# Optimization experiments

Hardware: AMD Instinct MI355X
Metric: run time of the kernel (lower is better)

Reference implementation:

```python
import jax, jax.numpy as jnp
import numpy as np

WSIZE = 8
HEADS = 6
CYC_SHIFT = True


def _relative_index(w):
    # same math as SelfAttention._getRelativeIndex
    coords = np.stack(np.meshgrid(np.arange(w), np.arange(w), indexing='ij'))
    coords = coords.reshape(2, -1)                      # [2, w*w]
    rel = coords[:, :, None] - coords[:, None, :]       # [2, N, N]
    rel = rel.copy()
    rel[0] += w - 1
    rel[0] *= 2 * w - 1
    rel[1] += w - 1
    return (rel[0] + rel[1]).reshape(-1)                # [N*N]


def _shift_mask(H, W, w):
    # same math as CycShftWndwPartition._mask
    part = np.zeros((H, W), dtype=np.float32)
    slices = [slice(0, -w), slice(-w, -w // 2), slice(-w // 2, None)]
    idx = 0
    for hs in slices:
        for ws_ in slices:
            part[hs, ws_] = idx
            idx += 1
    part = part.reshape(H // w, w, W // w, w).transpose(0, 2, 1, 3).reshape(-1, w * w)
    diff = part[:, None, :] - part[:, :, None]          # [nW, N, N]
    return np.where(diff != 0, -100.0, 0.0).astype(np.float32)


def setup_inputs() -> dict:
    key = jax.random.key(0)
    k0, k1, k2, k3, k4 = jax.random.split(key, 5)
    B, H, W, C = 4, 384, 384, 60
    return {
        'cvrt_img': jax.random.normal(k0, (B, H, W, C), dtype=jnp.float32),
        'qkv_w': jax.random.normal(k1, (C, 3 * C), dtype=jnp.float32) * 0.05,
        'bias_matrix': jax.random.normal(k2, ((2 * WSIZE - 1) ** 2, HEADS), dtype=jnp.float32) * 0.02,
        'proj_w': jax.random.normal(k3, (C, C), dtype=jnp.float32) * 0.05,
        'proj_b': jax.random.normal(k4, (C,), dtype=jnp.float32) * 0.02,
    }


def reference(cvrt_img, qkv_w, bias_matrix, proj_w, proj_b):
    B, H, W, C = cvrt_img.shape
    w = WSIZE
    N = w * w
    d = C // HEADS
    nWh, nWw = H // w, W // w
    WNum = nWh * nWw

    # cyclic shift + window partition
    if CYC_SHIFT:
        x = jnp.roll(cvrt_img, shift=(-(w // 2), -(w // 2)), axis=(1, 2))
        mask = jnp.asarray(_shift_mask(H, W, w))        # [WNum, N, N]
    else:
        x = cvrt_img
        mask = jnp.zeros((WNum, N, N), dtype=cvrt_img.dtype)
    windows = x.reshape(B, nWh, w, nWw, w, C).transpose(0, 1, 3, 2, 4, 5)
    windows = windows.reshape(B * WNum, N, C)

    # windowed multi-head self-attention
    qkv = (windows @ qkv_w).reshape(B * WNum, N, 3, HEADS, d)
    qkv = qkv.transpose(2, 0, 3, 1, 4)                  # [3, Bw, H, N, d]
    q, k, v = qkv[0], qkv[1], qkv[2]
    attn = jnp.einsum('bhnd,bhmd->bhnm', q, k) / (d ** 0.5)

    rel_idx = jnp.asarray(_relative_index(w))
    bias = bias_matrix[rel_idx].reshape(N, N, HEADS).transpose(2, 0, 1)  # [H, N, N]
    attn = attn + bias[None]

    attn = attn.reshape(B, WNum, HEADS, N, N) + mask[None, :, None]
    attn = jax.nn.softmax(attn.reshape(B * WNum, HEADS, N, N), axis=-1)

    out = jnp.einsum('bhnm,bhmd->bhnd', attn, v)        # [Bw, H, N, d]
    out = out.transpose(0, 2, 1, 3).reshape(B * WNum, N, C)
    new_windows = out @ proj_w + proj_b

    # un-partition + reverse cyclic shift
    y = new_windows.reshape(B, nWh, nWw, w, w, C).transpose(0, 1, 3, 2, 4, 5)
    y = y.reshape(B, H, W, C)
    if CYC_SHIFT:
        y = jnp.roll(y, shift=(w // 2, w // 2), axis=(1, 2))
    return y
```

## Files before the change

### kernel.cpp

```cpp
#include <hip/hip_runtime.h>
#include <hip/hip_bf16.h>

#define IMG    384
#define CDIM   60
#define NWIN   48
#define WNUM   (NWIN * NWIN)

typedef short  bf16x8 __attribute__((ext_vector_type(8)));
typedef float  f32x4  __attribute__((ext_vector_type(4)));
union Frag { int4 i4; bf16x8 b8; };

#define MFMA(a, b, c) __builtin_amdgcn_mfma_f32_16x16x32_bf16((a), (b), (c), 0, 0, 0)

#define WS_QKVF  0
#define WS_VF    24576
#define WS_PROJF 36864
#define WS_BIASC 45056

#define SCALE_L2E (0.31622776601683794f * 1.4426950408889634f)
#define MASK_L2E  144.26950408889634f
#define LOG2E     1.4426950408889634f

__device__ __forceinline__ unsigned short f2bf(float f) {
    unsigned int u = __float_as_uint(f);
    unsigned int r = u + 0x7fffu + ((u >> 16) & 1u);
    return (unsigned short)(r >> 16);
}
__device__ __forceinline__ unsigned int pk2bf(float a, float b) {
    union { __hip_bfloat162 h; unsigned int u; } c;
    c.h = __float22bfloat162_rn(float2{a, b});
    return c.u;
}
__device__ __forceinline__ int regionOf(int x) {
    return (x < IMG - 8) ? 0 : ((x < IMG - 4) ? 1 : 2);
}
__device__ __forceinline__ int swz(int row, int byteoff) {
    return (row * 128 + byteoff) ^ ((row & 7) << 4);
}
__device__ __forceinline__ int4 qk_frag(const unsigned short* buf, int tok, int h, int g) {
    if (g == 0) return *(const int4*)((const char*)buf + swz(tok, h * 16));
    if (g == 1) {
        int v = *(const int*)((const char*)buf + swz(tok, 96 + h * 4));
        return int4{v, 0, 0, 0};
    }
    return int4{0, 0, 0, 0};
}

template<int MC>
__device__ __forceinline__ void attn_group(
    int h, int m0, const Frag (&kb)[4],
    int lane, int l15, int g, int dl, bool boundary, int wh, int ww,
    const unsigned short* qall, const unsigned short* vall,
    unsigned short* osb,
    char* slab, int prow, const float4* biasC)
{
    Frag va[2];
    int vrow = (l15 < 10) ? h * 10 + l15 : 60;
    #pragma unroll
    for (int ks = 0; ks < 2; ++ks)
        va[ks].i4 = *(const int4*)((const char*)vall + swz(vrow, ks * 64 + g * 16));

    #pragma unroll
    for (int mm = 0; mm < MC; ++mm) {
        int m = m0 + mm;
        int i_tok = m * 16 + l15;
        Frag qa;
        qa.i4 = qk_frag(qall, i_tok, h, g);

        const float4* bc = biasC + (h * 16 + m * 4) * 64 + lane;
        f32x4 sacc[4];
        #pragma unroll
        for (int n = 0; n < 4; ++n) {
            float4 bb = bc[n * 64];
            f32x4 ci = {bb.x, bb.y, bb.z, bb.w};
            sacc[n] = MFMA(kb[n].b8, qa.b8, ci);
        }
        if (boundary) {
            int pi = regionOf(wh * 8 + (i_tok >> 3)) * 3 + regionOf(ww * 8 + (i_tok & 7));
            #pragma unroll
            for (int n = 0; n < 4; ++n)
                #pragma unroll
                for (int jj = 0; jj < 4; ++jj) {
                    int j = n * 16 + g * 4 + jj;
                    int pj = regionOf(wh * 8 + (j >> 3)) * 3 + regionOf(ww * 8 + (j & 7));
                    if (pi != pj) sacc[n][jj] -= MASK_L2E;
                }
        }
        unsigned w0[4], w1[4];
        #pragma unroll
        for (int n = 0; n < 4; ++n) {
            float e0 = __builtin_exp2f(sacc[n][0]);
            float e1 = __builtin_exp2f(sacc[n][1]);
            float e2 = __builtin_exp2f(sacc[n][2]);
            float e3 = __builtin_exp2f(sacc[n][3]);
            w0[n] = pk2bf(e0, e1);
            w1[n] = pk2bf(e2, e3);
        }
        f32x4 pv = {0.f, 0.f, 0.f, 0.f};
        *(int2*)(slab + swz(prow, 0 * 32 + g * 8)) = make_int2(w0[0], w1[0]);
        *(int2*)(slab + swz(prow, 1 * 32 + g * 8)) = make_int2(w0[1], w1[1]);
        {
            Frag pf;
            pf.i4 = *(const int4*)(slab + swz(prow, g * 16));
            pv = MFMA(va[0].b8, pf.b8, pv);
        }
        *(int2*)(slab + swz(prow, 0 * 32 + g * 8)) = make_int2(w0[2], w1[2]);
        *(int2*)(slab + swz(prow, 1 * 32 + g * 8)) = make_int2(w0[3], w1[3]);
        {
            Frag pf;
            pf.i4 = *(const int4*)(slab + swz(prow, g * 16));
            pv = MFMA(va[1].b8, pf.b8, pv);
        }
        float denom = __int_as_float(__builtin_amdgcn_ds_bpermute(dl, __float_as_int(pv[2])));
        float rinv  = __builtin_amdgcn_rcpf(denom);

        unsigned q01 = pk2bf(pv[0] * rinv, pv[1] * rinv);
        unsigned q23 = pk2bf(pv[2] * rinv, pv[3] * rinv);
        if (g < 2) {
            *(unsigned*)((char*)osb + swz(i_tok, h * 20 + g * 8 + 0)) = q01;
            *(unsigned*)((char*)osb + swz(i_tok, h * 20 + g * 8 + 4)) = q23;
        } else if (g == 2) {
            *(unsigned*)((char*)osb + swz(i_tok, h * 20 + 16)) = q01;
        }
    }
}

__global__ void swin_prep(const float* __restrict__ qw,
                          const float* __restrict__ pw,
                          const float* __restrict__ bias,
                          unsigned char* __restrict__ ws)
{
    int t = blockIdx.x * 256 + threadIdx.x;
    if (t < 1536) {
        int lane = t & 63, f = t >> 6;
        int mt = f >> 1, ks = f & 1;
        int h = mt >> 1, type = mt & 1;
        int d = lane & 15, g8 = lane >> 4;
        unsigned short v8[8];
        #pragma unroll
        for (int jj = 0; jj < 8; ++jj) {
            int c = ks * 32 + g8 * 8 + jj;
            float wv = (d < 10 && c < 60) ? qw[c * 180 + type * 60 + h * 10 + d] : 0.f;
            if (type == 0) wv *= SCALE_L2E;
            v8[jj] = f2bf(wv);
        }
        int4 p;
        p.x = v8[0] | (v8[1] << 16);  p.y = v8[2] | (v8[3] << 16);
        p.z = v8[4] | (v8[5] << 16);  p.w = v8[6] | (v8[7] << 16);
        *(int4*)(ws + WS_QKVF + t * 16) = p;
    } else if (t < 2304) {
        int t2 = t - 1536;
        int lane = t2 & 63, f = t2 >> 6;
        int h = f >> 1, ks = f & 1;
        int d = lane & 15, g8 = lane >> 4;
        unsigned short v8[8];
        #pragma unroll
        for (int jj = 0; jj < 8; ++jj) {
            int c = ks * 32 + g8 * 8 + jj;
            v8[jj] = f2bf((d < 10 && c < 60) ? qw[c * 180 + 120 + h * 10 + d] : 0.f);
        }
        int4 p;
        p.x = v8[0] | (v8[1] << 16);  p.y = v8[2] | (v8[3] << 16);
        p.z = v8[4] | (v8[5] << 16);  p.w = v8[6] | (v8[7] << 16);
        *(int4*)(ws + WS_VF + t2 * 16) = p;
    } else if (t < 2816) {
        int t2 = t - 2304;
        int lane = t2 & 63, fq = t2 >> 6;
        int m = fq >> 1, ks = fq & 1;
        int c = m * 16 + (lane & 15);
        int g8 = lane >> 4;
        unsigned short v8[8];
        #pragma unroll
        for (int jj = 0; jj < 8; ++jj) {
            int cc = ks * 32 + g8 * 8 + jj;
            v8[jj] = f2bf((c < 60 && cc < 60) ? pw[cc * 60 + c] : 0.f);
        }
        int4 p;
        p.x = v8[0] | (v8[1] << 16);  p.y = v8[2] | (v8[3] << 16);
        p.z = v8[4] | (v8[5] << 16);  p.w = v8[6] | (v8[7] << 16);
        *(int4*)(ws + WS_PROJF + t2 * 16) = p;
    } else if (t < 2816 + 24576) {
        int idx = t - 2816;
        int h = idx >> 12;
        int r = idx & 4095;
        int m = r >> 10;
        int n = (r >> 8) & 3;
        int lane = (r >> 2) & 63;
        int jj = r & 3;
        int i = m * 16 + (lane & 15);
        int j = n * 16 + (lane >> 4) * 4 + jj;
        int yi = i >> 3, xi = i & 7, yj = j >> 3, xj = j & 7;
        int ridx = (yi - yj + 7) * 15 + (xi - xj + 7);
        ((float*)(ws + WS_BIASC))[idx] = bias[ridx * 6 + h] * LOG2E;
    }
}

__global__ __launch_bounds__(256, 4)
void swin_mfma(const float* __restrict__ img,
               const float* __restrict__ pbias,
               const unsigned char* __restrict__ ws,
               float* __restrict__ out)
{
    __shared__ __align__(16) unsigned short uni [64 * 64];
    __shared__ __align__(16) unsigned short qall[64 * 64];
    __shared__ __align__(16) unsigned short kall[64 * 64];
    __shared__ __align__(16) unsigned short vall[61 * 64];

    const int tid  = threadIdx.x;
    const int lane = tid & 63;
    const int wid  = __builtin_amdgcn_readfirstlane(tid >> 6);
    const int l15  = lane & 15;
    const int g    = lane >> 4;
    const int dl   = (32 + l15) << 2;

    const int bid = blockIdx.x;
    const int b   = bid / WNUM;
    const int wi  = bid - b * WNUM;
    const int wh  = wi / NWIN;
    const int ww  = wi - wh * NWIN;
    const bool boundary = (wh == NWIN - 1) || (ww == NWIN - 1);

    {
        int tok = lane;
        int yi = tok >> 3, xi = tok & 7;
        int sh = wh * 8 + yi + 4; if (sh >= IMG) sh -= IMG;
        int sw = ww * 8 + xi + 4; if (sw >= IMG) sw -= IMG;
        const float* src = img + ((size_t)(b * IMG + sh) * IMG + sw) * CDIM;
        #pragma unroll
        for (int it = 0; it < 4; ++it) {
            int cg = wid + it * 4;
            if (cg < 15) {
                float4 v = *(const float4*)(src + cg * 4);
                *(int2*)((char*)uni + swz(tok, cg * 8)) =
                    make_int2(pk2bf(v.x, v.y), pk2bf(v.z, v.w));
            } else {
                *(int2*)((char*)uni + swz(tok, 120)) = make_int2(0, 0);
            }
        }
    }
    if (tid < 128) {
        int row = tid >> 1, half = tid & 1;
        *(unsigned int*)((char*)kall + swz(row, 120 + half * 4)) = 0u;
    }
    if (tid < 32) {
        *(unsigned int*)((char*)vall + swz(60, tid * 4)) = 0x3F803F80u;
    }
    __syncthreads();

    {
        Frag xb[4][2];
        #pragma unroll
        for (int n = 0; n < 4; ++n)
            #pragma unroll
            for (int ks = 0; ks < 2; ++ks)
                xb[n][ks].i4 = *(const int4*)((const char*)uni + swz(n * 16 + l15, ks * 64 + g * 16));

        const int4* wsq = (const int4*)(ws + WS_QKVF);
        #pragma unroll
        for (int kk = 0; kk < 3; ++kk) {
            int mt = wid + kk * 4;
            int h = mt >> 1, type = mt & 1;
            Frag a0, a1;
            a0.i4 = wsq[(mt * 2 + 0) * 64 + lane];
            a1.i4 = wsq[(mt * 2 + 1) * 64 + lane];
            unsigned short* dst = type ? kall : qall;
            #pragma unroll
            for (int n = 0; n < 4; ++n) {
                f32x4 acc = {0.f, 0.f, 0.f, 0.f};
                acc = MFMA(a0.b8, xb[n][0].b8, acc);
                acc = MFMA(a1.b8, xb[n][1].b8, acc);
                int tok = n * 16 + l15;
                unsigned pk01 = pk2bf(acc[0], acc[1]);
                unsigned pk23 = pk2bf(acc[2], acc[3]);
                if (g < 2)
                    *(int2*)((char*)dst + swz(tok, h * 16 + g * 8)) = make_int2(pk01, pk23);
                else if (g == 2)
                    *(unsigned*)((char*)dst + swz(tok, 96 + h * 4)) = pk01;
            }
        }
        const int4* wsv = (const int4*)(ws + WS_VF);
        int nv = (wid < 2) ? 2 : 1;
        #pragma unroll 1
        for (int kk = 0; kk < nv; ++kk) {
            int hv = wid + kk * 4;
            Frag b0, b1;
            b0.i4 = wsv[(hv * 2 + 0) * 64 + lane];
            b1.i4 = wsv[(hv * 2 + 1) * 64 + lane];
            #pragma unroll
            for (int n = 0; n < 4; ++n) {
                f32x4 acc = {0.f, 0.f, 0.f, 0.f};
                acc = MFMA(xb[n][0].b8, b0.b8, acc);
                acc = MFMA(xb[n][1].b8, b1.b8, acc);
                if (l15 < 10) {
                    *(int2*)((char*)vall + swz(hv * 10 + l15, n * 32 + g * 8)) =
                        make_int2(pk2bf(acc[0], acc[1]), pk2bf(acc[2], acc[3]));
                }
            }
        }
    }
    __syncthreads();

    {
        char* slab = (char*)uni;
        const int prow = wid * 16 + l15;
        const float4* biasC = (const float4*)(ws + WS_BIASC);
        const int h0 = wid + (wid >> 1);
        const int h1 = h0 + 1;

        Frag kb0[4], kb1[4];
        #pragma unroll
        for (int n = 0; n < 4; ++n) {
            kb0[n].i4 = qk_frag(kall, n * 16 + l15, h0, g);
            kb1[n].i4 = qk_frag(kall, n * 16 + l15, h1, g);
        }
        __syncthreads();

        if ((wid & 1) == 0) {
            attn_group<4>(h0, 0, kb0, lane, l15, g, dl, boundary, wh, ww,
                          qall, vall, kall, slab, prow, biasC);
            attn_group<2>(h1, 0, kb1, lane, l15, g, dl, boundary, wh, ww,
                          qall, vall, kall, slab, prow, biasC);
        } else {
            attn_group<2>(h0, 2, kb0, lane, l15, g, dl, boundary, wh, ww,
                          qall, vall, kall, slab, prow, biasC);
            attn_group<4>(h1, 0, kb1, lane, l15, g, dl, boundary, wh, ww,
                          qall, vall, kall, slab, prow, biasC);
        }
    }
    __syncthreads();

    {
        const int4* wsp = (const int4*)(ws + WS_PROJF);
        Frag a0, a1;
        a0.i4 = wsp[(wid * 2 + 0) * 64 + lane];
        a1.i4 = wsp[(wid * 2 + 1) * 64 + lane];
        int c0 = wid * 16 + g * 4;
        float4 pbv = (c0 < 60) ? *(const float4*)&pbias[c0] : float4{0.f, 0.f, 0.f, 0.f};
        #pragma unroll
        for (int n = 0; n < 4; ++n) {
            Frag b0, b1;
            b0.i4 = *(const int4*)((const char*)kall + swz(n * 16 + l15, g * 16));
            b1.i4 = *(const int4*)((const char*)kall + swz(n * 16 + l15, 64 + g * 16));
            f32x4 acc = {0.f, 0.f, 0.f, 0.f};
            acc = MFMA(a0.b8, b0.b8, acc);
            acc = MFMA(a1.b8, b1.b8, acc);
            if (c0 < 60) {
                int tok = n * 16 + l15;
                int yi = tok >> 3, xi = tok & 7;
                int sh = wh * 8 + yi + 4; if (sh >= IMG) sh -= IMG;
                int sw = ww * 8 + xi + 4; if (sw >= IMG) sw -= IMG;
                float4 o = {acc[0] + pbv.x, acc[1] + pbv.y, acc[2] + pbv.z, acc[3] + pbv.w};
                *(float4*)&out[((b * IMG + sh) * IMG + sw) * CDIM + c0] = o;
            }
        }
    }
}

extern "C" void kernel_launch(void* const* d_in, const int* in_sizes, int n_in,
                              void* d_out, int out_size, void* d_ws, size_t ws_size,
                              hipStream_t stream) {
    const float* img  = (const float*)d_in[0];
    const float* qw   = (const float*)d_in[1];
    const float* bias = (const float*)d_in[2];
    const float* pw   = (const float*)d_in[3];
    const float* pb   = (const float*)d_in[4];
    float* out = (float*)d_out;

    swin_prep<<<107, 256, 0, stream>>>(qw, pw, bias, (unsigned char*)d_ws);
    swin_mfma<<<4 * WNUM, 256, 0, stream>>>(img, pb,
                                            (const unsigned char*)d_ws, out);
}
```

Before: 163.5 us.

## Use 512-thread blocks with eight waves splitting work per window

Doubles the block size from 4 to 8 waves per window. Every stage (load, QKV projection, attention rows, output projection) is redistributed across the 8 waves, and the P slab is split into two halves so two groups of four waves can share the staging buffer. The aim is more parallelism per window and shorter per-wave serial chains. In exchange, per-wave register budgets are tighter under the new launch bounds, and the uneven split of head and row chunks may cause load imbalance.

After: 227.4 us. +39.1%, slower.

```diff
diff --git a/kernel.cpp b/kernel.cpp
--- a/kernel.cpp
+++ b/kernel.cpp
@@ -52,7 +52,7 @@
     int lane, int l15, int g, int dl, bool boundary, int wh, int ww,
     const unsigned short* qall, const unsigned short* vall,
     unsigned short* osb,
-    char* slab, int prow, const float4* biasC)
+    char* slab, int prow, int halfb, const float4* biasC)
 {
     Frag va[2];
     int vrow = (l15 < 10) ? h * 10 + l15 : 60;
@@ -97,18 +97,18 @@
             w1[n] = pk2bf(e2, e3);
         }
         f32x4 pv = {0.f, 0.f, 0.f, 0.f};
-        *(int2*)(slab + swz(prow, 0 * 32 + g * 8)) = make_int2(w0[0], w1[0]);
-        *(int2*)(slab + swz(prow, 1 * 32 + g * 8)) = make_int2(w0[1], w1[1]);
+        *(int2*)(slab + swz(prow, halfb + 0 * 32 + g * 8)) = make_int2(w0[0], w1[0]);
+        *(int2*)(slab + swz(prow, halfb + 1 * 32 + g * 8)) = make_int2(w0[1], w1[1]);
         {
             Frag pf;
-            pf.i4 = *(const int4*)(slab + swz(prow, g * 16));
+            pf.i4 = *(const int4*)(slab + swz(prow, halfb + g * 16));
             pv = MFMA(va[0].b8, pf.b8, pv);
         }
-        *(int2*)(slab + swz(prow, 0 * 32 + g * 8)) = make_int2(w0[2], w1[2]);
-        *(int2*)(slab + swz(prow, 1 * 32 + g * 8)) = make_int2(w0[3], w1[3]);
+        *(int2*)(slab + swz(prow, halfb + 0 * 32 + g * 8)) = make_int2(w0[2], w1[2]);
+        *(int2*)(slab + swz(prow, halfb + 1 * 32 + g * 8)) = make_int2(w0[3], w1[3]);
         {
             Frag pf;
-            pf.i4 = *(const int4*)(slab + swz(prow, g * 16));
+            pf.i4 = *(const int4*)(slab + swz(prow, halfb + g * 16));
             pv = MFMA(va[1].b8, pf.b8, pv);
         }
         float denom = __int_as_float(__builtin_amdgcn_ds_bpermute(dl, __float_as_int(pv[2])));
@@ -195,7 +195,7 @@
     }
 }
 
-__global__ __launch_bounds__(256, 4)
+__global__ __launch_bounds__(512, 6)
 void swin_mfma(const float* __restrict__ img,
                const float* __restrict__ pbias,
                const unsigned char* __restrict__ ws,
@@ -227,13 +227,13 @@
         int sw = ww * 8 + xi + 4; if (sw >= IMG) sw -= IMG;
         const float* src = img + ((size_t)(b * IMG + sh) * IMG + sw) * CDIM;
         #pragma unroll
-        for (int it = 0; it < 4; ++it) {
-            int cg = wid + it * 4;
+        for (int it = 0; it < 2; ++it) {
+            int cg = wid + it * 8;
             if (cg < 15) {
                 float4 v = *(const float4*)(src + cg * 4);
                 *(int2*)((char*)uni + swz(tok, cg * 8)) =
                     make_int2(pk2bf(v.x, v.y), pk2bf(v.z, v.w));
-            } else {
+            } else if (cg == 15) {
                 *(int2*)((char*)uni + swz(tok, 120)) = make_int2(0, 0);
             }
         }
@@ -256,9 +256,9 @@
                 xb[n][ks].i4 = *(const int4*)((const char*)uni + swz(n * 16 + l15, ks * 64 + g * 16));
 
         const int4* wsq = (const int4*)(ws + WS_QKVF);
-        #pragma unroll
-        for (int kk = 0; kk < 3; ++kk) {
-            int mt = wid + kk * 4;
+        const int4* wsv = (const int4*)(ws + WS_VF);
+
+        auto do_qk = [&](int mt) {
             int h = mt >> 1, type = mt & 1;
             Frag a0, a1;
             a0.i4 = wsq[(mt * 2 + 0) * 64 + lane];
@@ -277,12 +277,8 @@
                 else if (g == 2)
                     *(unsigned*)((char*)dst + swz(tok, 96 + h * 4)) = pk01;
             }
-        }
-        const int4* wsv = (const int4*)(ws + WS_VF);
-        int nv = (wid < 2) ? 2 : 1;
-        #pragma unroll 1
-        for (int kk = 0; kk < nv; ++kk) {
-            int hv = wid + kk * 4;
+        };
+        auto do_v = [&](int hv) {
             Frag b0, b1;
             b0.i4 = wsv[(hv * 2 + 0) * 64 + lane];
             b1.i4 = wsv[(hv * 2 + 1) * 64 + lane];
@@ -296,48 +292,72 @@
                         make_int2(pk2bf(acc[0], acc[1]), pk2bf(acc[2], acc[3]));
                 }
             }
+        };
+
+        if (wid < 4) {
+            do_qk(wid);
+            do_qk(8 + wid);
+        } else {
+            do_qk(wid);
+            do_v(wid - 4);
+            if (wid < 6) do_v(wid);
         }
     }
     __syncthreads();
 
     {
         char* slab = (char*)uni;
-        const int prow = wid * 16 + l15;
+        const int halfb = (wid >> 2) * 64;
+        const int prow  = (wid & 3) * 16 + l15;
         const float4* biasC = (const float4*)(ws + WS_BIASC);
-        const int h0 = wid + (wid >> 1);
-        const int h1 = h0 + 1;
-
-        Frag kb0[4], kb1[4];
+        const int hbase = (wid >> 2) * 3;
+        const int wq = wid & 3;
+
+        int hA, hB;
+        if (wq == 0)      { hA = hbase;     hB = hbase;     }
+        else if (wq == 1) { hA = hbase;     hB = hbase + 1; }
+        else if (wq == 2) { hA = hbase + 1; hB = hbase + 2; }
+        else              { hA = hbase + 2; hB = hbase + 2; }
+
+        Frag kbA[4], kbB[4];
         #pragma unroll
         for (int n = 0; n < 4; ++n) {
-            kb0[n].i4 = qk_frag(kall, n * 16 + l15, h0, g);
-            kb1[n].i4 = qk_frag(kall, n * 16 + l15, h1, g);
+            kbA[n].i4 = qk_frag(kall, n * 16 + l15, hA, g);
+            kbB[n].i4 = qk_frag(kall, n * 16 + l15, hB, g);
         }
         __syncthreads();
 
-        if ((wid & 1) == 0) {
-            attn_group<4>(h0, 0, kb0, lane, l15, g, dl, boundary, wh, ww,
-                          qall, vall, kall, slab, prow, biasC);
-            attn_group<2>(h1, 0, kb1, lane, l15, g, dl, boundary, wh, ww,
-                          qall, vall, kall, slab, prow, biasC);
+        if (wq == 0) {
+            attn_group<3>(hA, 0, kbA, lane, l15, g, dl, boundary, wh, ww,
+                          qall, vall, kall, slab, prow, halfb, biasC);
+        } else if (wq == 1) {
+            attn_group<1>(hA, 3, kbA, lane, l15, g, dl, boundary, wh, ww,
+                          qall, vall, kall, slab, prow, halfb, biasC);
+            attn_group<2>(hB, 0, kbB, lane, l15, g, dl, boundary, wh, ww,
+                          qall, vall, kall, slab, prow, halfb, biasC);
+        } else if (wq == 2) {
+            attn_group<2>(hA, 2, kbA, lane, l15, g, dl, boundary, wh, ww,
+                          qall, vall, kall, slab, prow, halfb, biasC);
+            attn_group<1>(hB, 0, kbB, lane, l15, g, dl, boundary, wh, ww,
+                          qall, vall, kall, slab, prow, halfb, biasC);
         } else {
-            attn_group<2>(h0, 2, kb0, lane, l15, g, dl, boundary, wh, ww,
-                          qall, vall, kall, slab, prow, biasC);
-            attn_group<4>(h1, 0, kb1, lane, l15, g, dl, boundary, wh, ww,
-                          qall, vall, kall, slab, prow, biasC);
+            attn_group<3>(hA, 1, kbA, lane, l15, g, dl, boundary, wh, ww,
+                          qall, vall, kall, slab, prow, halfb, biasC);
         }
     }
     __syncthreads();
 
     {
         const int4* wsp = (const int4*)(ws + WS_PROJF);
+        int mt = wid >> 1, nh = wid & 1;
         Frag a0, a1;
-        a0.i4 = wsp[(wid * 2 + 0) * 64 + lane];
-        a1.i4 = wsp[(wid * 2 + 1) * 64 + lane];
-        int c0 = wid * 16 + g * 4;
+        a0.i4 = wsp[(mt * 2 + 0) * 64 + lane];
+        a1.i4 = wsp[(mt * 2 + 1) * 64 + lane];
+        int c0 = mt * 16 + g * 4;
         float4 pbv = (c0 < 60) ? *(const float4*)&pbias[c0] : float4{0.f, 0.f, 0.f, 0.f};
         #pragma unroll
-        for (int n = 0; n < 4; ++n) {
+        for (int nn = 0; nn < 2; ++nn) {
+            int n = nh * 2 + nn;
             Frag b0, b1;
             b0.i4 = *(const int4*)((const char*)kall + swz(n * 16 + l15, g * 16));
             b1.i4 = *(const int4*)((const char*)kall + swz(n * 16 + l15, 64 + g * 16));
@@ -367,6 +387,6 @@
     float* out = (float*)d_out;
 
     swin_prep<<<107, 256, 0, stream>>>(qw, pw, bias, (unsigned char*)d_ws);
-    swin_mfma<<<4 * WNUM, 256, 0, stream>>>(img, pb,
+    swin_mfma<<<4 * WNUM, 512, 0, stream>>>(img, pb,
                                             (const unsigned char*)d_ws, out);
 }
```
